# Kernel tuning notes

Measured on AMD Instinct MI355X. Metric: run time of the kernel, lower is better.

## Reference

```python
import jax, jax.numpy as jnp
import numpy as np

HIDDEN_DIM = 256
NLAT, NLON = 64, 128
BATCH, N_STATIONS = 2, 1024


def _grid_coords():
    lat = jnp.linspace(-90.0, 90.0, NLAT)
    lon = jnp.linspace(-180.0, 180.0, NLON)
    lat_mesh, lon_mesh = jnp.meshgrid(lat, lon, indexing='ij')
    return lat_mesh.reshape(-1), lon_mesh.reshape(-1)  # (n_grid,)


def setup_inputs() -> dict:
    key = jax.random.key(0)
    k1, k2, k3, k4, k5, k6 = jax.random.split(key, 6)
    station_features = jax.random.normal(k1, (BATCH, N_STATIONS, HIDDEN_DIM), dtype=jnp.float32)
    station_coords = jax.random.normal(k2, (BATCH, N_STATIONS, 3), dtype=jnp.float32)
    mask = jnp.ones((BATCH, N_STATIONS), dtype=jnp.float32)
    # distance_mlp params: Linear(3,32) -> GELU -> Linear(32,1) -> Softplus
    W1 = jax.random.normal(k3, (3, 32), dtype=jnp.float32) * (1.0 / np.sqrt(3.0))
    b1 = jax.random.normal(k4, (32,), dtype=jnp.float32) * 0.02
    W2 = jax.random.normal(k5, (32, 1), dtype=jnp.float32) * (1.0 / np.sqrt(32.0))
    b2 = jax.random.normal(k6, (1,), dtype=jnp.float32) * 0.02
    return {"station_features": station_features, "station_coords": station_coords,
            "mask": mask, "W1": W1, "b1": b1, "W2": W2, "b2": b2}


def reference(station_features, station_coords, mask, W1, b1, W2, b2):
    lat_grid, lon_grid = _grid_coords()  # (G,)
    station_lat = station_coords[:, :, 0]  # (B,S)
    station_lon = station_coords[:, :, 1]
    dlat = station_lat[:, :, None] - lat_grid[None, None, :]  # (B,S,G)
    dlon = station_lon[:, :, None] - lon_grid[None, None, :]
    dist = jnp.sqrt(dlat**2 + dlon**2 + 1e-6)
    dist_features = jnp.stack([dist, dlat, dlon], axis=-1)  # (B,S,G,3)
    h = jax.nn.gelu(dist_features @ W1 + b1, approximate=False)  # (B,S,G,32)
    weights = jax.nn.softplus((h @ W2 + b2)[..., 0])  # (B,S,G)
    weights = weights * mask[:, :, None]
    weights = jax.nn.softmax(weights, axis=1)  # over stations
    grid = jnp.einsum('bsg,bsd->bgd', weights, station_features)
    grid = grid.reshape(station_features.shape[0], NLAT, NLON, HIDDEN_DIM)
    return jnp.transpose(grid, (0, 3, 1, 2))  # (B, D, nlat, nlon)
```

## Files before the change

### kernel.cpp

```cpp
#include <hip/hip_runtime.h>
#include <math.h>

#define NLAT 64
#define NLON 128
#define HID  256
#define NSTA 1024
#define TG   16
#define SC   128
#define NCHUNK (NSTA / SC)
#define NGRP 16
#define TABN 4096
#define TABW 4.5f

#define LOG2E 1.4426950408889634f
#define LN2   0.69314718055994531f

typedef float f32x4 __attribute__((ext_vector_type(4)));
typedef _Float16 f16x8 __attribute__((ext_vector_type(8)));
typedef _Float16 f16x4 __attribute__((ext_vector_type(4)));

__device__ __forceinline__ float gelu_ref(float x) {
    const float p  = 0.3275911f;
    const float a1 = 0.254829592f, a2 = -0.284496736f, a3 = 1.421413741f,
                a4 = -1.453152027f, a5 = 1.061405429f;
    float z  = x * 0.70710678118654752f;
    float az = fabsf(z);
    float t  = __builtin_amdgcn_rcpf(fmaf(p, az, 1.0f));
    float poly = fmaf(fmaf(fmaf(fmaf(a5, t, a4), t, a3), t, a2), t, a1) * t;
    float e  = __builtin_amdgcn_exp2f(az * az * -LOG2E);
    float r  = fmaf(-poly, e, 1.0f);
    float erfz = copysignf(r, z);
    float hx = 0.5f * x;
    return fmaf(hx, erfz, hx);
}

__global__ __launch_bounds__(256)
void cvt_kernel(const float* __restrict__ feats, _Float16* __restrict__ fhi,
                _Float16* __restrict__ flo) {
    __shared__ float tile[16][64];
    const int blk = blockIdx.x;
    const int b  = blk >> 8;
    const int st = (blk >> 2) & 63;
    const int dt = blk & 3;
    {
        const int s  = threadIdx.x >> 4;
        const int dq = threadIdx.x & 15;
        const float4 vv = *(const float4*)
            &feats[((size_t)(b * NSTA + st * 16 + s)) * HID + dt * 64 + dq * 4];
        *(float4*)&tile[s][dq * 4] = vv;
    }
    __syncthreads();
    const int d  = threadIdx.x >> 2;
    const int sq = threadIdx.x & 3;
    f16x4 hi4, lo4;
#pragma unroll
    for (int k = 0; k < 4; ++k) {
        float v = tile[sq * 4 + k][d];
        _Float16 h = (_Float16)v;
        hi4[k] = h;
        lo4[k] = (_Float16)(v - (float)h);
    }
    const size_t o = ((size_t)(b * HID + dt * 64 + d)) * NSTA + st * 16 + sq * 4;
    *(f16x4*)&fhi[o] = hi4;
    *(f16x4*)&flo[o] = lo4;
}

__global__ __launch_bounds__(256, 4)
void s2g_kernel(const float* __restrict__ coords,
                const float* __restrict__ maskp,
                const float* __restrict__ W1,
                const float* __restrict__ b1,
                const float* __restrict__ W2,
                const float* __restrict__ b2p,
                const _Float16* __restrict__ fhi,
                const _Float16* __restrict__ flo,
                float* __restrict__ out)
{
    __shared__ float gtab[TABN];
    __shared__ __align__(16) f16x8 fragAh[256];
    __shared__ __align__(16) f16x8 fragAl[256];
    __shared__ __align__(16) float slat[SC], slon[SC], smask[SC];
    __shared__ float4 wpack[32];
    __shared__ float w2s[32];
    __shared__ __align__(16) float maxbuf[NGRP * TG], psum[NGRP * TG];
    __shared__ __align__(16) float mS[TG], lS[TG], alphaS[TG];

    const int tid  = threadIdx.x;
    const int blk  = blockIdx.x & 511;
    const int b    = blockIdx.x >> 9;
    const int lat  = blk >> 3;
    const int lon0 = (blk & 7) * TG;

    const float latv = -90.0f + (180.0f / 63.0f) * (float)lat;

    const float TH = 2.0f * TABW / (float)TABN;
#pragma unroll
    for (int k = tid; k < TABN; k += 256) {
        float x = -TABW + ((float)k + 0.5f) * TH;
        gtab[k] = gelu_ref(x) - fmaxf(x, 0.0f);
    }
    if (tid < 32) {
        wpack[tid] = make_float4(W1[tid], W1[32 + tid], W1[64 + tid], b1[tid]);
        w2s[tid]   = W2[tid];
        if (tid < TG) { mS[tid] = -1.0e30f; lS[tid] = 0.0f; }
    }
    const float b2 = b2p[0];

    const int gA   = tid & (TG - 1);
    const int sgrp = tid >> 4;
    const float lonvA = -180.0f + (360.0f / 127.0f) * (float)(lon0 + gA);

    const int lane = tid & 63;
    const int wv   = tid >> 6;

    f32x4 acc[4];
#pragma unroll
    for (int t = 0; t < 4; ++t) acc[t] = (f32x4){0.0f, 0.0f, 0.0f, 0.0f};

    const float* cbase = coords + (size_t)b * NSTA * 3;
    const float* mbase = maskp  + (size_t)b * NSTA;
    const _Float16* fhb = fhi + (size_t)b * HID * NSTA;
    const _Float16* flb = flo + (size_t)b * HID * NSTA;

    const float ISCALE = (float)TABN / (2.0f * TABW);
    const float IOFF   = (float)TABN * 0.5f;

    for (int c = 0; c < NCHUNK; ++c) {
        const int s0 = c * SC;
        __syncthreads();
        if (tid < SC) {
            slat[tid]  = cbase[(size_t)(s0 + tid) * 3 + 0];
            slon[tid]  = cbase[(size_t)(s0 + tid) * 3 + 1];
            smask[tid] = mbase[s0 + tid];
        }
        __syncthreads();

        float dist[8], dlat[8], dlon[8], v[8];
#pragma unroll
        for (int i = 0; i < 8; ++i) {
            int s = sgrp * 8 + i;
            float dla = slat[s] - latv;
            float dlo = slon[s] - lonvA;
            dlat[i] = dla;
            dlon[i] = dlo;
            dist[i] = sqrtf(fmaf(dla, dla, fmaf(dlo, dlo, 1e-6f)));
            v[i] = b2;
        }
#pragma unroll 2
        for (int j = 0; j < 32; ++j) {
            float4 wj = wpack[j];
            float  w2 = w2s[j];
#pragma unroll
            for (int i = 0; i < 8; ++i) {
                float pre = fmaf(wj.x, dist[i], fmaf(wj.y, dlat[i], fmaf(wj.z, dlon[i], wj.w)));
                float cl  = fminf(fmaxf(pre, -TABW), 4.4999f);
                int  idx  = (int)fmaf(cl, ISCALE, IOFF);
                float r   = gtab[idx];
                v[i] = fmaf(w2, fmaxf(pre, 0.0f), v[i]);
                v[i] = fmaf(w2, r, v[i]);
            }
        }
        float lmax = -3.0e38f;
#pragma unroll
        for (int i = 0; i < 8; ++i) {
            int s = sgrp * 8 + i;
            float x  = v[i];
            float ax = fabsf(x);
            float e  = __builtin_amdgcn_exp2f(-ax * LOG2E);
            float sp = fmaxf(x, 0.0f) + __builtin_amdgcn_logf(1.0f + e) * LN2;
            v[i] = sp * smask[s];
            lmax = fmaxf(lmax, v[i]);
        }
        maxbuf[sgrp * TG + gA] = lmax;
        __syncthreads();

        if (tid < TG) {
            float cm = maxbuf[tid];
#pragma unroll
            for (int k = 1; k < NGRP; ++k) cm = fmaxf(cm, maxbuf[k * TG + tid]);
            float mold = mS[tid];
            float mnew = fmaxf(mold, cm);
            alphaS[tid] = __builtin_amdgcn_exp2f((mold - mnew) * LOG2E);
            mS[tid] = mnew;
        }
        __syncthreads();

        {
            float m  = mS[gA];
            float ps = 0.0f;
            f16x8 fh, fl;
#pragma unroll
            for (int i = 0; i < 8; ++i) {
                float p = __builtin_amdgcn_exp2f((v[i] - m) * LOG2E);
                _Float16 h = (_Float16)p;
                fh[i] = h;
                fl[i] = (_Float16)(p - (float)h);
                ps += p;
            }
            const int idx = ((sgrp >> 2) << 6) + (((sgrp & 3) << 4) | gA);
            fragAh[idx] = fh;
            fragAl[idx] = fl;
            psum[sgrp * TG + gA] = ps;
        }
        __syncthreads();

        if (tid < TG) {
            float t = 0.0f;
#pragma unroll
            for (int k = 0; k < NGRP; ++k) t += psum[k * TG + tid];
            lS[tid] = lS[tid] * alphaS[tid] + t;
        }

        {
            const f32x4 al = *(const f32x4*)&alphaS[(lane >> 4) * 4];
#pragma unroll
            for (int t = 0; t < 4; ++t) acc[t] = acc[t] * al;

            const int srow = s0 + ((lane >> 4) * 8);
            const int dbase = wv * 64 + (lane & 15);
#pragma unroll
            for (int kc = 0; kc < 4; ++kc) {
                f16x8 ah = fragAh[(kc << 6) + lane];
                f16x8 al16 = fragAl[(kc << 6) + lane];
#pragma unroll
                for (int t = 0; t < 4; ++t) {
                    const size_t off = (size_t)(dbase + t * 16) * NSTA + srow + kc * 32;
                    f16x8 bh = *(const f16x8*)(fhb + off);
                    f16x8 bl = *(const f16x8*)(flb + off);
                    acc[t] = __builtin_amdgcn_mfma_f32_16x16x32_f16(ah, bh, acc[t], 0, 0, 0);
                    acc[t] = __builtin_amdgcn_mfma_f32_16x16x32_f16(ah, bl, acc[t], 0, 0, 0);
                    acc[t] = __builtin_amdgcn_mfma_f32_16x16x32_f16(al16, bh, acc[t], 0, 0, 0);
                }
            }
        }
    }
    __syncthreads();

    {
        const float4 l4 = *(const float4*)&lS[(lane >> 4) * 4];
        const float4 rl = make_float4(1.0f / l4.x, 1.0f / l4.y, 1.0f / l4.z, 1.0f / l4.w);
        const int m0 = (lane >> 4) * 4;
        const size_t gbase = (size_t)lat * NLON + lon0 + m0;
#pragma unroll
        for (int t = 0; t < 4; ++t) {
            const int d = wv * 64 + t * 16 + (lane & 15);
            float4 o;
            o.x = acc[t].x * rl.x;
            o.y = acc[t].y * rl.y;
            o.z = acc[t].z * rl.z;
            o.w = acc[t].w * rl.w;
            *reinterpret_cast<float4*>(out + ((size_t)(b * HID + d)) * (NLAT * NLON) + gbase) = o;
        }
    }
}

extern "C" void kernel_launch(void* const* d_in, const int* in_sizes, int n_in,
                              void* d_out, int out_size, void* d_ws, size_t ws_size,
                              hipStream_t stream) {
    const float* feats  = (const float*)d_in[0];
    const float* coords = (const float*)d_in[1];
    const float* maskp  = (const float*)d_in[2];
    const float* W1     = (const float*)d_in[3];
    const float* b1     = (const float*)d_in[4];
    const float* W2     = (const float*)d_in[5];
    const float* b2     = (const float*)d_in[6];
    float* out          = (float*)d_out;

    _Float16* fhi = (_Float16*)d_ws;
    _Float16* flo = fhi + (size_t)2 * HID * NSTA;

    hipLaunchKernelGGL(cvt_kernel, dim3(512), dim3(256), 0, stream, feats, fhi, flo);
    hipLaunchKernelGGL(s2g_kernel, dim3(1024), dim3(256), 0, stream,
                       coords, maskp, W1, b1, W2, b2, fhi, flo, out);
}
```

Measured before the change: 248.0 us.

## Double station chunk with 512-thread blocks, split-K MFMA, drop weight lo-part

The station chunk size grows from 128 to 256 and blocks from 256 to 512 threads. The eight waves split the K (station) dimension into two halves and reduce their partial accumulators through shared memory at the end. The fp16 low-part correction of the softmax weights is dropped, which cuts the MFMAs per tile from three to two but lowers the precision of the weights. The conversion kernel also now handles 64 stations per block with wider stores, and the GELU table term is folded into one FMA.

```diff
diff --git a/kernel.cpp b/kernel.cpp
--- a/kernel.cpp
+++ b/kernel.cpp
@@ -6,9 +6,9 @@
 #define HID  256
 #define NSTA 1024
 #define TG   16
-#define SC   128
+#define SC   256
 #define NCHUNK (NSTA / SC)
-#define NGRP 16
+#define NGRP 32
 #define TABN 4096
 #define TABW 4.5f
 
@@ -17,7 +17,6 @@
 
 typedef float f32x4 __attribute__((ext_vector_type(4)));
 typedef _Float16 f16x8 __attribute__((ext_vector_type(8)));
-typedef _Float16 f16x4 __attribute__((ext_vector_type(4)));
 
 __device__ __forceinline__ float gelu_ref(float x) {
     const float p  = 0.3275911f;
@@ -37,35 +36,41 @@
 __global__ __launch_bounds__(256)
 void cvt_kernel(const float* __restrict__ feats, _Float16* __restrict__ fhi,
                 _Float16* __restrict__ flo) {
-    __shared__ float tile[16][64];
+    __shared__ float tile[64][68];
     const int blk = blockIdx.x;
-    const int b  = blk >> 8;
-    const int st = (blk >> 2) & 63;
+    const int b  = blk >> 6;
+    const int st = (blk >> 2) & 15;
     const int dt = blk & 3;
     {
-        const int s  = threadIdx.x >> 4;
         const int dq = threadIdx.x & 15;
-        const float4 vv = *(const float4*)
-            &feats[((size_t)(b * NSTA + st * 16 + s)) * HID + dt * 64 + dq * 4];
-        *(float4*)&tile[s][dq * 4] = vv;
+        const int sr = threadIdx.x >> 4;
+#pragma unroll
+        for (int k = 0; k < 4; ++k) {
+            int s = k * 16 + sr;
+            float4 vv = *(const float4*)
+                &feats[((size_t)(b * NSTA + st * 64 + s)) * HID + dt * 64 + dq * 4];
+            *(float4*)&tile[s][dq * 4] = vv;
+        }
     }
     __syncthreads();
     const int d  = threadIdx.x >> 2;
-    const int sq = threadIdx.x & 3;
-    f16x4 hi4, lo4;
-#pragma unroll
-    for (int k = 0; k < 4; ++k) {
-        float v = tile[sq * 4 + k][d];
+    const int sg = threadIdx.x & 3;
+    f16x8 h8[2], l8[2];
+#pragma unroll
+    for (int k = 0; k < 16; ++k) {
+        float v = tile[sg * 16 + k][d];
         _Float16 h = (_Float16)v;
-        hi4[k] = h;
-        lo4[k] = (_Float16)(v - (float)h);
-    }
-    const size_t o = ((size_t)(b * HID + dt * 64 + d)) * NSTA + st * 16 + sq * 4;
-    *(f16x4*)&fhi[o] = hi4;
-    *(f16x4*)&flo[o] = lo4;
-}
-
-__global__ __launch_bounds__(256, 4)
+        h8[k >> 3][k & 7] = h;
+        l8[k >> 3][k & 7] = (_Float16)(v - (float)h);
+    }
+    const size_t o = ((size_t)(b * HID + dt * 64 + d)) * NSTA + st * 64 + sg * 16;
+    *(f16x8*)&fhi[o]     = h8[0];
+    *(f16x8*)&fhi[o + 8] = h8[1];
+    *(f16x8*)&flo[o]     = l8[0];
+    *(f16x8*)&flo[o + 8] = l8[1];
+}
+
+__global__ __launch_bounds__(512, 8)
 void s2g_kernel(const float* __restrict__ coords,
                 const float* __restrict__ maskp,
                 const float* __restrict__ W1,
@@ -76,9 +81,8 @@
                 const _Float16* __restrict__ flo,
                 float* __restrict__ out)
 {
-    __shared__ float gtab[TABN];
-    __shared__ __align__(16) f16x8 fragAh[256];
-    __shared__ __align__(16) f16x8 fragAl[256];
+    __shared__ __align__(16) float gtab[TABN];
+    __shared__ __align__(16) f16x8 fragAh[512];
     __shared__ __align__(16) float slat[SC], slon[SC], smask[SC];
     __shared__ float4 wpack[32];
     __shared__ float w2s[32];
@@ -95,7 +99,7 @@
 
     const float TH = 2.0f * TABW / (float)TABN;
 #pragma unroll
-    for (int k = tid; k < TABN; k += 256) {
+    for (int k = tid; k < TABN; k += 512) {
         float x = -TABW + ((float)k + 0.5f) * TH;
         gtab[k] = gelu_ref(x) - fmaxf(x, 0.0f);
     }
@@ -112,6 +116,8 @@
 
     const int lane = tid & 63;
     const int wv   = tid >> 6;
+    const int kc0  = (wv >> 2) * 4;
+    const int dsel = (wv & 3) * 64;
 
     f32x4 acc[4];
 #pragma unroll
@@ -155,9 +161,8 @@
                 float pre = fmaf(wj.x, dist[i], fmaf(wj.y, dlat[i], fmaf(wj.z, dlon[i], wj.w)));
                 float cl  = fminf(fmaxf(pre, -TABW), 4.4999f);
                 int  idx  = (int)fmaf(cl, ISCALE, IOFF);
-                float r   = gtab[idx];
-                v[i] = fmaf(w2, fmaxf(pre, 0.0f), v[i]);
-                v[i] = fmaf(w2, r, v[i]);
+                float ge  = fmaxf(pre, 0.0f) + gtab[idx];
+                v[i] = fmaf(w2, ge, v[i]);
             }
         }
         float lmax = -3.0e38f;
@@ -188,18 +193,14 @@
         {
             float m  = mS[gA];
             float ps = 0.0f;
-            f16x8 fh, fl;
+            f16x8 fh;
 #pragma unroll
             for (int i = 0; i < 8; ++i) {
                 float p = __builtin_amdgcn_exp2f((v[i] - m) * LOG2E);
-                _Float16 h = (_Float16)p;
-                fh[i] = h;
-                fl[i] = (_Float16)(p - (float)h);
+                fh[i] = (_Float16)p;
                 ps += p;
             }
-            const int idx = ((sgrp >> 2) << 6) + (((sgrp & 3) << 4) | gA);
-            fragAh[idx] = fh;
-            fragAl[idx] = fl;
+            fragAh[((sgrp >> 2) << 6) + (((sgrp & 3) << 4) | gA)] = fh;
             psum[sgrp * TG + gA] = ps;
         }
         __syncthreads();
@@ -216,20 +217,19 @@
 #pragma unroll
             for (int t = 0; t < 4; ++t) acc[t] = acc[t] * al;
 
-            const int srow = s0 + ((lane >> 4) * 8);
-            const int dbase = wv * 64 + (lane & 15);
+            const int srow = (lane >> 4) * 8;
+            const int dbase = dsel + (lane & 15);
 #pragma unroll
             for (int kc = 0; kc < 4; ++kc) {
-                f16x8 ah = fragAh[(kc << 6) + lane];
-                f16x8 al16 = fragAl[(kc << 6) + lane];
+                f16x8 a = fragAh[((kc0 + kc) << 6) + lane];
 #pragma unroll
                 for (int t = 0; t < 4; ++t) {
-                    const size_t off = (size_t)(dbase + t * 16) * NSTA + srow + kc * 32;
+                    const size_t off = (size_t)(dbase + t * 16) * NSTA +
+                                       s0 + (kc0 + kc) * 32 + srow;
                     f16x8 bh = *(const f16x8*)(fhb + off);
                     f16x8 bl = *(const f16x8*)(flb + off);
-                    acc[t] = __builtin_amdgcn_mfma_f32_16x16x32_f16(ah, bh, acc[t], 0, 0, 0);
-                    acc[t] = __builtin_amdgcn_mfma_f32_16x16x32_f16(ah, bl, acc[t], 0, 0, 0);
-                    acc[t] = __builtin_amdgcn_mfma_f32_16x16x32_f16(al16, bh, acc[t], 0, 0, 0);
+                    acc[t] = __builtin_amdgcn_mfma_f32_16x16x32_f16(a, bh, acc[t], 0, 0, 0);
+                    acc[t] = __builtin_amdgcn_mfma_f32_16x16x32_f16(a, bl, acc[t], 0, 0, 0);
                 }
             }
         }
@@ -237,19 +237,28 @@
     __syncthreads();
 
     {
-        const float4 l4 = *(const float4*)&lS[(lane >> 4) * 4];
-        const float4 rl = make_float4(1.0f / l4.x, 1.0f / l4.y, 1.0f / l4.z, 1.0f / l4.w);
-        const int m0 = (lane >> 4) * 4;
-        const size_t gbase = (size_t)lat * NLON + lon0 + m0;
-#pragma unroll
-        for (int t = 0; t < 4; ++t) {
-            const int d = wv * 64 + t * 16 + (lane & 15);
-            float4 o;
-            o.x = acc[t].x * rl.x;
-            o.y = acc[t].y * rl.y;
-            o.z = acc[t].z * rl.z;
-            o.w = acc[t].w * rl.w;
-            *reinterpret_cast<float4*>(out + ((size_t)(b * HID + d)) * (NLAT * NLON) + gbase) = o;
+        f32x4* red = reinterpret_cast<f32x4*>(gtab);
+        if (wv >= 4) {
+#pragma unroll
+            for (int t = 0; t < 4; ++t) red[(((wv & 3) * 4 + t) << 6) + lane] = acc[t];
+        }
+        __syncthreads();
+        if (wv < 4) {
+            const float4 l4 = *(const float4*)&lS[(lane >> 4) * 4];
+            const float4 rl = make_float4(1.0f / l4.x, 1.0f / l4.y, 1.0f / l4.z, 1.0f / l4.w);
+            const int m0 = (lane >> 4) * 4;
+            const size_t gbase = (size_t)lat * NLON + lon0 + m0;
+#pragma unroll
+            for (int t = 0; t < 4; ++t) {
+                f32x4 s = acc[t] + red[((wv * 4 + t) << 6) + lane];
+                const int d = dsel + t * 16 + (lane & 15);
+                float4 o;
+                o.x = s.x * rl.x;
+                o.y = s.y * rl.y;
+                o.z = s.z * rl.z;
+                o.w = s.w * rl.w;
+                *reinterpret_cast<float4*>(out + ((size_t)(b * HID + d)) * (NLAT * NLON) + gbase) = o;
+            }
         }
     }
 }
@@ -269,7 +278,7 @@
     _Float16* fhi = (_Float16*)d_ws;
     _Float16* flo = fhi + (size_t)2 * HID * NSTA;
 
-    hipLaunchKernelGGL(cvt_kernel, dim3(512), dim3(256), 0, stream, feats, fhi, flo);
-    hipLaunchKernelGGL(s2g_kernel, dim3(1024), dim3(256), 0, stream,
+    hipLaunchKernelGGL(cvt_kernel, dim3(128), dim3(256), 0, stream, feats, fhi, flo);
+    hipLaunchKernelGGL(s2g_kernel, dim3(1024), dim3(512), 0, stream,
                        coords, maskp, W1, b1, W2, b2, fhi, flo, out);
 }
```

Result: slower. 274.8 us (+10.8%).
